# Kernel tuning notes

Hardware: AMD Instinct MI355X
Metric: run time of the kernel (lower is better)

The kernel has to match this reference:

```python
import jax, jax.numpy as jnp
import numpy as np

NS, B, PH = 8, 1024, 12
XS, ZS, RNN = 256, 32, 512
LS, LPS = 8, 2           # len_state, len_pred_state
IN = LPS + ZS + XS       # GRU input size (include_robot=False)
DT = 0.4                 # SingleIntegrator dt


def setup_inputs() -> dict:
    key = jax.random.key(0)
    ks = jax.random.split(key, 16)
    g = lambda k, sh, s=0.05: jax.random.normal(k, sh, dtype=jnp.float32) * s
    N = NS * B
    return {
        "x": g(ks[0], (B, XS), 1.0),
        "x_r_t0": g(ks[1], (B, LS), 1.0),
        "z_stacked": g(ks[2], (NS, B, ZS), 1.0),
        "p0": g(ks[3], (B, 2), 1.0),
        "eps_step": g(ks[4], (PH, N, 2), 1.0),
        "eps_final": g(ks[5], (NS, B, PH, 2), 1.0),
        "W_sa": g(ks[6], (LPS, LS)), "b_sa": jnp.zeros((LPS,), jnp.float32),
        "W_ih": g(ks[7], (3 * RNN, IN)), "b_ih": jnp.zeros((3 * RNN,), jnp.float32),
        "W_hh": g(ks[8], (3 * RNN, RNN)), "b_hh": jnp.zeros((3 * RNN,), jnp.float32),
        "W_h0": g(ks[9], (RNN, ZS + XS)), "b_h0": jnp.zeros((RNN,), jnp.float32),
        "W_mu": g(ks[10], (LPS, RNN)), "b_mu": jnp.zeros((LPS,), jnp.float32),
        "W_ls": g(ks[11], (LPS, RNN), 0.01), "b_ls": jnp.zeros((LPS,), jnp.float32),
        "W_corr": g(ks[12], (1, RNN), 0.01), "b_corr": jnp.zeros((1,), jnp.float32),
        "prediction_horizon": PH,
        "n_samples": NS,
    }


def _gmm_sample(mus, log_sigmas, rho, eps):
    # Reparameterized sample from a single-component 2D correlated Gaussian:
    # a = mu + L @ eps with L = [[sx, 0], [sy*rho, sy*sqrt(1-rho^2)]]
    s = jnp.exp(log_sigmas)
    dx = s[..., 0] * eps[..., 0]
    dy = s[..., 1] * (rho * eps[..., 0]
                      + jnp.sqrt(jnp.clip(1.0 - rho * rho, 1e-5, None)) * eps[..., 1])
    return mus + jnp.stack([dx, dy], axis=-1)


def reference(x, x_r_t0, z_stacked, p0, eps_step, eps_final,
              W_sa, b_sa, W_ih, b_ih, W_hh, b_hh, W_h0, b_h0,
              W_mu, b_mu, W_ls, b_ls, W_corr, b_corr,
              prediction_horizon, n_samples):
    ns, bsz, zs = z_stacked.shape
    z = z_stacked.reshape(-1, zs)                               # [N, z]
    zx = jnp.concatenate([z, jnp.tile(x, (n_samples, 1))], axis=1)  # [N, z+x]
    state0 = zx @ W_h0.T + b_h0                                 # initial_h
    a0 = jnp.tile(x_r_t0 @ W_sa.T + b_sa, (n_samples, 1))       # state_action

    def step(carry, eps_t):
        h, a = carry
        inp = jnp.concatenate([zx, a], axis=1)                  # [N, IN]
        gi = inp @ W_ih.T + b_ih
        gh = h @ W_hh.T + b_hh
        ir, iz, inn = jnp.split(gi, 3, axis=1)
        hr, hz, hn = jnp.split(gh, 3, axis=1)
        r = jax.nn.sigmoid(ir + hr)
        u = jax.nn.sigmoid(iz + hz)
        n = jnp.tanh(inn + r * hn)
        h_new = (1.0 - u) * n + u * h                           # GRUCell
        mus = h_new @ W_mu.T + b_mu                             # [N, 2]
        log_sigmas = h_new @ W_ls.T + b_ls                      # [N, 2]
        corrs = jnp.tanh(h_new @ W_corr.T + b_corr)[:, 0]       # [N]
        a_t = _gmm_sample(mus, log_sigmas, corrs, eps_t)        # gmm.rsample()
        return (h_new, a_t), (mus, log_sigmas, corrs)

    _, (mus, log_sigmas, corrs) = jax.lax.scan(step, (state0, a0), eps_step)
    # [PH, N, .] -> [n_samples, B, PH, .]  (n_components == 1)
    mus = mus.transpose(1, 0, 2).reshape(n_samples, bsz, prediction_horizon, 2)
    log_sigmas = log_sigmas.transpose(1, 0, 2).reshape(n_samples, bsz, prediction_horizon, 2)
    corrs = corrs.transpose(1, 0).reshape(n_samples, bsz, prediction_horizon, 1)
    log_pis = jnp.ones_like(corrs)                              # ones_like path (n_components==1)

    # a_dist.rsample() then SingleIntegrator.integrate_samples
    a_sample = _gmm_sample(mus, log_sigmas, corrs[..., 0], eps_final)
    preds = jnp.cumsum(a_sample, axis=2) * DT + p0[None, :, None, :]
    return (log_pis, mus, log_sigmas, corrs, preds)
```

## Files before the change

kernel.cpp:

```cpp
#include <hip/hip_runtime.h>
#include <hip/hip_bf16.h>
#include <math.h>

#define NSAMP 8
#define BATCH 1024
#define PH 12
#define XS 256
#define ZS 32
#define RNN 512
#define LSZ 8
#define INP 290
#define NTOT 8192
#define DT 0.4f

#define LOGPI_OFF 0
#define MUS_OFF   (NTOT*PH)
#define LSIG_OFF  (MUS_OFF + NTOT*PH*2)
#define CORR_OFF  (LSIG_OFF + NTOT*PH*2)
#define PRED_OFF  (CORR_OFF + NTOT*PH)

typedef float f32x4 __attribute__((ext_vector_type(4)));
typedef __bf16 bf16x8 __attribute__((ext_vector_type(8)));

__device__ __forceinline__ float sigmoid_(float x) {
    return 1.0f / (1.0f + __expf(-x));
}
__device__ __forceinline__ float tanh_(float x) {
    return 1.0f - 2.0f / (__expf(2.0f * x) + 1.0f);
}
__device__ __forceinline__ unsigned short f2bfu(float v) {
    __hip_bfloat16 b = __float2bfloat16(v);
    return __builtin_bit_cast(unsigned short, b);
}

__device__ __forceinline__ void async16(const void* g, void* l) {
    __builtin_amdgcn_global_load_lds((const __attribute__((address_space(1))) void*)g,
                                     (__attribute__((address_space(3))) void*)l, 16, 0, 0);
}


__global__ void k_init_a(const float* __restrict__ x_r_t0,
                         const float* __restrict__ W_sa,
                         const float* __restrict__ b_sa,
                         float* __restrict__ a) {
    int n = blockIdx.x * blockDim.x + threadIdx.x;
    if (n >= NTOT) return;
    int b = n & (BATCH - 1);
    float a0 = b_sa[0], a1 = b_sa[1];
#pragma unroll
    for (int k = 0; k < LSZ; ++k) {
        float xv = x_r_t0[b * LSZ + k];
        a0 = fmaf(xv, W_sa[0 * LSZ + k], a0);
        a1 = fmaf(xv, W_sa[1 * LSZ + k], a1);
    }
    a[n * 2 + 0] = a0;
    a[n * 2 + 1] = a1;
}

__global__ void k_cast_zx(const float* __restrict__ z, const float* __restrict__ x,
                          __hip_bfloat16* __restrict__ zx) {
    int n = blockIdx.x, k = threadIdx.x;
    if (k >= 288) return;
    float v = (k < 32) ? z[n * ZS + k] : x[(n & (BATCH - 1)) * XS + (k - 32)];
    zx[(size_t)n * 288 + k] = __float2bfloat16(v);
}

__global__ void k_cast_w(const float* __restrict__ W_h0, const float* __restrict__ W_ih,
                         __hip_bfloat16* __restrict__ Wcat) {
    int r = blockIdx.x, k = threadIdx.x;
    if (k >= 288) return;
    float v = (r < RNN) ? W_h0[r * 288 + k] : W_ih[(size_t)(r - RNN) * INP + k];
    Wcat[(size_t)r * 288 + k] = __float2bfloat16(v);
}

__global__ void k_cast_whh(const float* __restrict__ W, __hip_bfloat16* __restrict__ Wb) {
    int i = blockIdx.x * 256 + threadIdx.x;
    Wb[i] = __float2bfloat16(W[i]);
}

__global__ __launch_bounds__(256, 2) void k_gemm0_mfma(
    const __hip_bfloat16* __restrict__ zx, const __hip_bfloat16* __restrict__ Wcat,
    const float* __restrict__ b_h0, const float* __restrict__ b_ih,
    __hip_bfloat16* __restrict__ h0, unsigned short* __restrict__ giP)
{
    __shared__ __align__(16) char sA[8192];
    __shared__ __align__(16) char sB[8192];
    const int tid = threadIdx.x;
    const int wv = tid >> 6, lane = tid & 63;
    const int fq = lane >> 4, fr = lane & 15;
    const int wr = wv >> 1, wc = wv & 1;
    const int tile_r = blockIdx.x * 128, tile_c = blockIdx.y * 128;

    f32x4 acc[4][4];
#pragma unroll
    for (int i = 0; i < 4; ++i)
#pragma unroll
        for (int j = 0; j < 4; ++j) acc[i][j] = (f32x4){0.f, 0.f, 0.f, 0.f};

    for (int k0 = 0; k0 < 288; k0 += 32) {
#pragma unroll
        for (int j = 0; j < 2; ++j) {
            int ck = wv * 2 + j;
            int row = ck * 16 + (lane >> 2);
            int slot = lane & 3;
            async16(zx + (size_t)(tile_r + row) * 288 + k0 + ((slot ^ (row & 3)) << 3),
                    sA + ck * 1024 + lane * 16);
        }
#pragma unroll
        for (int j = 0; j < 2; ++j) {
            int ck = wv * 2 + j;
            int row = ck * 16 + (lane >> 2);
            int slot = lane & 3;
            async16(Wcat + (size_t)(tile_c + row) * 288 + k0 + ((slot ^ (row & 3)) << 3),
                    sB + ck * 1024 + lane * 16);
        }
        __syncthreads();
        bf16x8 af[4], bv[4];
#pragma unroll
        for (int i = 0; i < 4; ++i) {
            int r = wr * 64 + i * 16 + fr;
            af[i] = *(const bf16x8*)(sA + r * 64 + ((fq ^ (r & 3)) << 4));
        }
#pragma unroll
        for (int j = 0; j < 4; ++j) {
            int r = wc * 64 + j * 16 + fr;
            bv[j] = *(const bf16x8*)(sB + r * 64 + ((fq ^ (r & 3)) << 4));
        }
#pragma unroll
        for (int i = 0; i < 4; ++i)
#pragma unroll
            for (int j = 0; j < 4; ++j)
                acc[i][j] = __builtin_amdgcn_mfma_f32_16x16x32_bf16(af[i], bv[j], acc[i][j], 0, 0, 0);
        __syncthreads();
    }

#pragma unroll
    for (int jn = 0; jn < 4; ++jn) {
        const int cg_full = tile_c + wc * 64 + jn * 16 + fr;
        if (cg_full < RNN) {
            const float bias = b_h0[cg_full];
#pragma unroll
            for (int i = 0; i < 4; ++i)
#pragma unroll
                for (int q = 0; q < 4; ++q) {
                    int rg = tile_r + wr * 64 + i * 16 + fq * 4 + q;
                    h0[(size_t)rg * RNN + cg_full] = __float2bfloat16(acc[i][jn][q] + bias);
                }
        } else {
            const int cp = cg_full - RNN;
            const float bias = b_ih[cp];
            const int g = cp >> 9;
            const int cgm = cp & 511;
            const int by = cgm >> 6;
            const int wcg = (cgm >> 5) & 1;
            const int jg = (cgm >> 4) & 1;
            const int frg = cgm & 15;
#pragma unroll
            for (int i = 0; i < 4; ++i) {
                const int rg = tile_r + wr * 64 + i * 16 + fq * 4;
                const int bxg = rg >> 8;
                const int r255 = rg & 255;
                const int wrg = r255 >> 6;
                const int ig = (r255 >> 4) & 3;
                const int fqg = (r255 >> 2) & 3;
                const int tidg = (wrg * 2 + wcg) * 64 + fqg * 16 + frg;
                const size_t base = ((size_t)(bxg * 8 + by) * 512 + tidg) * 96
                                    + (jg * 3 + g) * 16 + ig * 4;
                ushort4 pk;
                pk.x = f2bfu(acc[i][jn][0] + bias);
                pk.y = f2bfu(acc[i][jn][1] + bias);
                pk.z = f2bfu(acc[i][jn][2] + bias);
                pk.w = f2bfu(acc[i][jn][3] + bias);
                *reinterpret_cast<ushort4*>(giP + base) = pk;
            }
        }
    }
}

#define GRU_LDS_A 32768
#define GRU_LDS_BUF 57344
__global__ __launch_bounds__(512, 2) void k_gru_step_mfma(
    const __hip_bfloat16* __restrict__ h, const float* __restrict__ a,
    const unsigned short* __restrict__ giP,
    const __hip_bfloat16* __restrict__ Whh, const float* __restrict__ b_hh,
    const float* __restrict__ W_ih,
    __hip_bfloat16* __restrict__ h_new)
{
    __shared__ __align__(16) char lds[2][GRU_LDS_BUF];
    const int tid = threadIdx.x;
    const int wv = tid >> 6, lane = tid & 63;
    const int fq = lane >> 4, fr = lane & 15;
    const int wr = wv >> 1, wc = wv & 1;
    const int tile_r = blockIdx.x * 256;
    const int tile_c = blockIdx.y * 64;

    const unsigned short* pg = giP + ((size_t)(blockIdx.x * 8 + blockIdx.y) * 512 + tid) * 96;
    bf16x8 gv[12];
#pragma unroll
    for (int e = 0; e < 12; ++e)
        gv[e] = *reinterpret_cast<const bf16x8*>(pg + e * 8);

    f32x4 acc[3][4][2];
#pragma unroll
    for (int g = 0; g < 3; ++g)
#pragma unroll
        for (int i = 0; i < 4; ++i)
#pragma unroll
            for (int j = 0; j < 2; ++j) acc[g][i][j] = (f32x4){0.f, 0.f, 0.f, 0.f};

    const int lrow = lane >> 2;
    const int slot = (lane & 3) ^ (lrow & 3);

    auto stage = [&](int b, int k0) {
#pragma unroll
        for (int j = 0; j < 7; ++j) {
            int c = wv * 7 + j;
            if (c < 32) {
                int rowgrp = c >> 1, kh = c & 1;
                int row = tile_r + rowgrp * 16 + lrow;
                async16(h + (size_t)row * RNN + k0 + kh * 32 + slot * 8,
                        lds[b] + c * 1024 + lane * 16);
            } else {
                int cp = c - 32;
                int grp = cp >> 1, kh = cp & 1;
                int rB = grp * 16 + lrow;
                int gate = rB >> 6, col = rB & 63;
                async16(Whh + (size_t)(gate * RNN + tile_c + col) * RNN + k0 + kh * 32 + slot * 8,
                        lds[b] + GRU_LDS_A + cp * 1024 + lane * 16);
            }
        }
    };

    auto compute = [&](int b) {
        const char* bufA = lds[b];
        const char* bufB = lds[b] + GRU_LDS_A;
        const int rsw = (fq ^ (fr & 3)) << 4;
#pragma unroll
        for (int ks = 0; ks < 2; ++ks) {
            bf16x8 af[4];
#pragma unroll
            for (int i = 0; i < 4; ++i) {
                int chunk = (wr * 4 + i) * 2 + ks;
                af[i] = *(const bf16x8*)(bufA + chunk * 1024 + fr * 64 + rsw);
            }
            bf16x8 bv[3][2];
#pragma unroll
            for (int g = 0; g < 3; ++g)
#pragma unroll
                for (int j = 0; j < 2; ++j) {
                    int grp = g * 4 + wc * 2 + j;
                    int chunk = grp * 2 + ks;
                    bv[g][j] = *(const bf16x8*)(bufB + chunk * 1024 + fr * 64 + rsw);
                }
#pragma unroll
            for (int g = 0; g < 3; ++g)
#pragma unroll
                for (int i = 0; i < 4; ++i)
#pragma unroll
                    for (int j = 0; j < 2; ++j)
                        acc[g][i][j] = __builtin_amdgcn_mfma_f32_16x16x32_bf16(
                            af[i], bv[g][j], acc[g][i][j], 0, 0, 0);
        }
    };

    stage(0, 0);
    __syncthreads();
    int buf = 0;
#pragma unroll 1
    for (int t = 0; t < 7; ++t) {
        stage(buf ^ 1, (t + 1) * 64);
        compute(buf);
        __syncthreads();
        buf ^= 1;
    }
    compute(buf);

#pragma unroll
    for (int j = 0; j < 2; ++j) {
        const int cg = tile_c + wc * 32 + j * 16 + fr;
        const float bh_r = b_hh[cg], bh_z = b_hh[RNN + cg], bh_n = b_hh[2 * RNN + cg];
        const float wr0 = W_ih[(size_t)cg * INP + 288],             wr1 = W_ih[(size_t)cg * INP + 289];
        const float wz0 = W_ih[(size_t)(RNN + cg) * INP + 288],     wz1 = W_ih[(size_t)(RNN + cg) * INP + 289];
        const float wn0 = W_ih[(size_t)(2 * RNN + cg) * INP + 288], wn1 = W_ih[(size_t)(2 * RNN + cg) * INP + 289];
#pragma unroll
        for (int i = 0; i < 4; ++i)
#pragma unroll
            for (int q = 0; q < 4; ++q) {
                const int rg = tile_r + wr * 64 + i * 16 + fq * 4 + q;
                const int idx = i * 4 + q;
                const int half = idx >> 3, lidx = idx & 7;
                const float2 av = *(const float2*)&a[rg * 2];
                const float gr = __bfloat162float(gv[(j * 3 + 0) * 2 + half][lidx])
                                 + av.x * wr0 + av.y * wr1 + acc[0][i][j][q] + bh_r;
                const float gz = __bfloat162float(gv[(j * 3 + 1) * 2 + half][lidx])
                                 + av.x * wz0 + av.y * wz1 + acc[1][i][j][q] + bh_z;
                const float gn = __bfloat162float(gv[(j * 3 + 2) * 2 + half][lidx])
                                 + av.x * wn0 + av.y * wn1;
                const float r_ = sigmoid_(gr);
                const float u_ = sigmoid_(gz);
                const float n_ = tanh_(gn + r_ * (acc[2][i][j][q] + bh_n));
                const float hv = __bfloat162float(h[(size_t)rg * RNN + cg]);
                h_new[(size_t)rg * RNN + cg] = __float2bfloat16((1.0f - u_) * n_ + u_ * hv);
            }
    }
}

__global__ __launch_bounds__(256) void k_heads(
    const __hip_bfloat16* __restrict__ h_new,
    const float* __restrict__ W_mu, const float* __restrict__ b_mu,
    const float* __restrict__ W_ls, const float* __restrict__ b_ls,
    const float* __restrict__ W_corr, const float* __restrict__ b_corr,
    const float* __restrict__ eps_step_t,
    float* __restrict__ out, float* __restrict__ a, int t)
{
    const int wid = (blockIdx.x * blockDim.x + threadIdx.x) >> 6;
    const int lane = threadIdx.x & 63;
    if (wid >= NTOT) return;
    const int kbase = lane * 8;
    float hv[8];
    {
        uint4 v = *reinterpret_cast<const uint4*>(&h_new[(size_t)wid * RNN + kbase]);
        unsigned uu[4] = {v.x, v.y, v.z, v.w};
#pragma unroll
        for (int p = 0; p < 4; ++p) {
            hv[2 * p]     = __uint_as_float(uu[p] << 16);
            hv[2 * p + 1] = __uint_as_float(uu[p] & 0xffff0000u);
        }
    }
    float s0 = 0.f, s1 = 0.f, s2 = 0.f, s3 = 0.f, s4 = 0.f;
#pragma unroll
    for (int q = 0; q < 8; ++q) {
        int k = kbase + q;
        s0 = fmaf(hv[q], W_mu[k], s0);
        s1 = fmaf(hv[q], W_mu[RNN + k], s1);
        s2 = fmaf(hv[q], W_ls[k], s2);
        s3 = fmaf(hv[q], W_ls[RNN + k], s3);
        s4 = fmaf(hv[q], W_corr[k], s4);
    }
#pragma unroll
    for (int m = 32; m >= 1; m >>= 1) {
        s0 += __shfl_xor(s0, m, 64);
        s1 += __shfl_xor(s1, m, 64);
        s2 += __shfl_xor(s2, m, 64);
        s3 += __shfl_xor(s3, m, 64);
        s4 += __shfl_xor(s4, m, 64);
    }
    if (lane == 0) {
        const int n = wid;
        const float mu0 = s0 + b_mu[0], mu1 = s1 + b_mu[1];
        const float ls0 = s2 + b_ls[0], ls1 = s3 + b_ls[1];
        const float rho = tanh_(s4 + b_corr[0]);
        out[MUS_OFF + (n * PH + t) * 2 + 0] = mu0;
        out[MUS_OFF + (n * PH + t) * 2 + 1] = mu1;
        out[LSIG_OFF + (n * PH + t) * 2 + 0] = ls0;
        out[LSIG_OFF + (n * PH + t) * 2 + 1] = ls1;
        out[CORR_OFF + n * PH + t] = rho;
        const float e0 = eps_step_t[n * 2 + 0], e1 = eps_step_t[n * 2 + 1];
        const float sg0 = __expf(ls0), sg1 = __expf(ls1);
        a[n * 2 + 0] = mu0 + sg0 * e0;
        a[n * 2 + 1] = mu1 + sg1 * (rho * e0 + sqrtf(fmaxf(1e-5f, 1.0f - rho * rho)) * e1);
    }
}

__global__ void k_final(const float* __restrict__ p0,
                        const float* __restrict__ eps_final,
                        float* __restrict__ out)
{
    int n = blockIdx.x * blockDim.x + threadIdx.x;
    if (n >= NTOT) return;
    const int b = n & (BATCH - 1);
    const float px = p0[b * 2 + 0], py = p0[b * 2 + 1];
    float cx = 0.f, cy = 0.f;
#pragma unroll
    for (int t = 0; t < PH; ++t) {
        const float mu0 = out[MUS_OFF + (n * PH + t) * 2 + 0];
        const float mu1 = out[MUS_OFF + (n * PH + t) * 2 + 1];
        const float ls0 = out[LSIG_OFF + (n * PH + t) * 2 + 0];
        const float ls1 = out[LSIG_OFF + (n * PH + t) * 2 + 1];
        const float rho = out[CORR_OFF + n * PH + t];
        const float e0 = eps_final[(n * PH + t) * 2 + 0];
        const float e1 = eps_final[(n * PH + t) * 2 + 1];
        const float sg0 = __expf(ls0), sg1 = __expf(ls1);
        cx += mu0 + sg0 * e0;
        cy += mu1 + sg1 * (rho * e0 + sqrtf(fmaxf(1e-5f, 1.0f - rho * rho)) * e1);
        out[PRED_OFF + (n * PH + t) * 2 + 0] = cx * DT + px;
        out[PRED_OFF + (n * PH + t) * 2 + 1] = cy * DT + py;
        out[LOGPI_OFF + n * PH + t] = 1.0f;
    }
}

extern "C" void kernel_launch(void* const* d_in, const int* in_sizes, int n_in,
                              void* d_out, int out_size, void* d_ws, size_t ws_size,
                              hipStream_t stream) {
    const float* x        = (const float*)d_in[0];
    const float* x_r_t0   = (const float*)d_in[1];
    const float* z        = (const float*)d_in[2];
    const float* p0       = (const float*)d_in[3];
    const float* eps_step = (const float*)d_in[4];
    const float* eps_fin  = (const float*)d_in[5];
    const float* W_sa     = (const float*)d_in[6];
    const float* b_sa     = (const float*)d_in[7];
    const float* W_ih     = (const float*)d_in[8];
    const float* b_ih     = (const float*)d_in[9];
    const float* W_hh     = (const float*)d_in[10];
    const float* b_hh     = (const float*)d_in[11];
    const float* W_h0     = (const float*)d_in[12];
    const float* b_h0     = (const float*)d_in[13];
    const float* W_mu     = (const float*)d_in[14];
    const float* b_mu     = (const float*)d_in[15];
    const float* W_ls     = (const float*)d_in[16];
    const float* b_ls     = (const float*)d_in[17];
    const float* W_corr   = (const float*)d_in[18];
    const float* b_corr   = (const float*)d_in[19];

    char* wp = (char*)d_ws;
    float* a            = (float*)wp;          wp += (size_t)NTOT * 2 * 4;
    __hip_bfloat16* zxb = (__hip_bfloat16*)wp; wp += (size_t)NTOT * 288 * 2;
    __hip_bfloat16* Wcat= (__hip_bfloat16*)wp; wp += (size_t)2048 * 288 * 2;
    __hip_bfloat16* Whhb= (__hip_bfloat16*)wp; wp += (size_t)1536 * RNN * 2;
    __hip_bfloat16* h0  = (__hip_bfloat16*)wp; wp += (size_t)NTOT * RNN * 2;
    __hip_bfloat16* h1  = (__hip_bfloat16*)wp; wp += (size_t)NTOT * RNN * 2;
    unsigned short* giP = (unsigned short*)wp; wp += (size_t)NTOT * 1536 * 2;
    float* out = (float*)d_out;

    k_init_a<<<dim3(NTOT / 256), dim3(256), 0, stream>>>(x_r_t0, W_sa, b_sa, a);
    k_cast_zx<<<dim3(NTOT), dim3(320), 0, stream>>>(z, x, zxb);
    k_cast_w<<<dim3(2048), dim3(320), 0, stream>>>(W_h0, W_ih, Wcat);
    k_cast_whh<<<dim3(1536 * RNN / 256), dim3(256), 0, stream>>>(W_hh, Whhb);
    k_gemm0_mfma<<<dim3(64, 16), dim3(256), 0, stream>>>(zxb, Wcat, b_h0, b_ih, h0, giP);

    __hip_bfloat16* hc = h0;
    __hip_bfloat16* hn = h1;
    for (int t = 0; t < PH; ++t) {
        k_gru_step_mfma<<<dim3(NTOT / 256, RNN / 64), dim3(512), 0, stream>>>(
            hc, a, giP, Whhb, b_hh, W_ih, hn);
        k_heads<<<dim3(NTOT * 64 / 256), dim3(256), 0, stream>>>(
            hn, W_mu, b_mu, W_ls, b_ls, W_corr, b_corr,
            eps_step + (size_t)t * NTOT * 2, out, a, t);
        __hip_bfloat16* tmp = hc; hc = hn; hn = tmp;
    }
    k_final<<<dim3(NTOT / 256), dim3(256), 0, stream>>>(p0, eps_fin, out);
}
```

Measured before the change: 426.0 us.

## Restructure GRU step K-loop with deeper prefetch and explicit waitcnt barriers

Replaces the double-buffered __syncthreads loop in the GRU MFMA step kernel with a fully unrolled loop. Two stages are prefetched ahead, LDS fragments are read into registers before a barrier so the freed buffer can be refilled early, and explicit vmcnt/lgkmcnt waits replace full syncs. MFMA issue is wrapped in s_setprio, and the gate-input register loads move after the GEMM loop to lower register pressure during it. This relies on the hand-set vmcnt(7) matching the per-thread load count (7 async loads per stage), which may be fragile. Holding all fragments in registers also raises register use.

Result: slower. 480.6 us (+12.8%).

```diff
diff --git a/kernel.cpp b/kernel.cpp
--- a/kernel.cpp
+++ b/kernel.cpp
@@ -21,6 +21,12 @@
 
 typedef float f32x4 __attribute__((ext_vector_type(4)));
 typedef __bf16 bf16x8 __attribute__((ext_vector_type(8)));
+
+#define ASM_VMCNT7() asm volatile("s_waitcnt vmcnt(7)" ::: "memory")
+#define ASM_VMCNT0() asm volatile("s_waitcnt vmcnt(0)" ::: "memory")
+#define ASM_LGKM0()  asm volatile("s_waitcnt lgkmcnt(0)" ::: "memory")
+#define SBAR()       __builtin_amdgcn_s_barrier()
+#define SCHEDB()     __builtin_amdgcn_sched_barrier(0)
 
 __device__ __forceinline__ float sigmoid_(float x) {
     return 1.0f / (1.0f + __expf(-x));
@@ -194,12 +200,6 @@
     const int tile_r = blockIdx.x * 256;
     const int tile_c = blockIdx.y * 64;
 
-    const unsigned short* pg = giP + ((size_t)(blockIdx.x * 8 + blockIdx.y) * 512 + tid) * 96;
-    bf16x8 gv[12];
-#pragma unroll
-    for (int e = 0; e < 12; ++e)
-        gv[e] = *reinterpret_cast<const bf16x8*>(pg + e * 8);
-
     f32x4 acc[3][4][2];
 #pragma unroll
     for (int g = 0; g < 3; ++g)
@@ -231,27 +231,34 @@
         }
     };
 
-    auto compute = [&](int b) {
+    bf16x8 af[4][2];
+    bf16x8 bv[3][2][2];
+    const int rsw = (fq ^ (fr & 3)) << 4;
+
+    auto ldsread = [&](int b) {
         const char* bufA = lds[b];
         const char* bufB = lds[b] + GRU_LDS_A;
-        const int rsw = (fq ^ (fr & 3)) << 4;
 #pragma unroll
         for (int ks = 0; ks < 2; ++ks) {
-            bf16x8 af[4];
 #pragma unroll
             for (int i = 0; i < 4; ++i) {
                 int chunk = (wr * 4 + i) * 2 + ks;
-                af[i] = *(const bf16x8*)(bufA + chunk * 1024 + fr * 64 + rsw);
+                af[i][ks] = *(const bf16x8*)(bufA + chunk * 1024 + fr * 64 + rsw);
             }
-            bf16x8 bv[3][2];
 #pragma unroll
             for (int g = 0; g < 3; ++g)
 #pragma unroll
                 for (int j = 0; j < 2; ++j) {
                     int grp = g * 4 + wc * 2 + j;
                     int chunk = grp * 2 + ks;
-                    bv[g][j] = *(const bf16x8*)(bufB + chunk * 1024 + fr * 64 + rsw);
+                    bv[g][j][ks] = *(const bf16x8*)(bufB + chunk * 1024 + fr * 64 + rsw);
                 }
+        }
+    };
+
+    auto domfma = [&]() {
+#pragma unroll
+        for (int ks = 0; ks < 2; ++ks)
 #pragma unroll
             for (int g = 0; g < 3; ++g)
 #pragma unroll
@@ -259,21 +266,38 @@
 #pragma unroll
                     for (int j = 0; j < 2; ++j)
                         acc[g][i][j] = __builtin_amdgcn_mfma_f32_16x16x32_bf16(
-                            af[i], bv[g][j], acc[g][i][j], 0, 0, 0);
-        }
+                            af[i][ks], bv[g][j][ks], acc[g][i][j], 0, 0, 0);
     };
 
     stage(0, 0);
-    __syncthreads();
-    int buf = 0;
-#pragma unroll 1
-    for (int t = 0; t < 7; ++t) {
-        stage(buf ^ 1, (t + 1) * 64);
-        compute(buf);
-        __syncthreads();
-        buf ^= 1;
-    }
-    compute(buf);
+    stage(1, 64);
+    ASM_VMCNT7();
+    SBAR();
+    SCHEDB();
+
+#pragma unroll
+    for (int t = 0; t < 8; ++t) {
+        ldsread(t & 1);
+        ASM_LGKM0();
+        SCHEDB();
+        SBAR();
+        if (t + 2 < 8) stage(t & 1, (t + 2) * 64);
+        __builtin_amdgcn_s_setprio(1);
+        domfma();
+        __builtin_amdgcn_s_setprio(0);
+        if (t < 7) {
+            if (t + 2 < 8) ASM_VMCNT7();
+            else           ASM_VMCNT0();
+            SBAR();
+            SCHEDB();
+        }
+    }
+
+    const unsigned short* pg = giP + ((size_t)(blockIdx.x * 8 + blockIdx.y) * 512 + tid) * 96;
+    bf16x8 gv[12];
+#pragma unroll
+    for (int e = 0; e < 12; ++e)
+        gv[e] = *reinterpret_cast<const bf16x8*>(pg + e * 8);
 
 #pragma unroll
     for (int j = 0; j < 2; ++j) {
```

## Deepen GRU-step prefetch pipeline, double-buffer gemm0, and merge prep kernels

Applied to the files above, without the earlier changes.

The GRU step kernel now stages two K-tiles ahead and uses explicit vmcnt/lgkmcnt waits with raw barriers in place of full __syncthreads. It also defers the giP gate-input loads until after the matmul loop, which frees registers during the main loop. The initial gemm0 kernel gains double-buffered LDS so the next tile loads while the current one computes. The four small prep/cast kernels are merged into two to cut launch overhead. The hand-placed waitcnt logic is fragile if the number of outstanding loads per thread changes.

Result: slower. 485.0 us (+13.8%).

```diff
diff --git a/kernel.cpp b/kernel.cpp
--- a/kernel.cpp
+++ b/kernel.cpp
@@ -22,6 +22,11 @@
 typedef float f32x4 __attribute__((ext_vector_type(4)));
 typedef __bf16 bf16x8 __attribute__((ext_vector_type(8)));
 
+#define ASM_VMCNT7() asm volatile("s_waitcnt vmcnt(7)" ::: "memory")
+#define ASM_VMCNT0() asm volatile("s_waitcnt vmcnt(0)" ::: "memory")
+#define ASM_LGKM0()  asm volatile("s_waitcnt lgkmcnt(0)" ::: "memory")
+#define SBAR()       __builtin_amdgcn_s_barrier()
+
 __device__ __forceinline__ float sigmoid_(float x) {
     return 1.0f / (1.0f + __expf(-x));
 }
@@ -38,44 +43,41 @@
                                      (__attribute__((address_space(3))) void*)l, 16, 0, 0);
 }
 
-
-__global__ void k_init_a(const float* __restrict__ x_r_t0,
-                         const float* __restrict__ W_sa,
-                         const float* __restrict__ b_sa,
-                         float* __restrict__ a) {
-    int n = blockIdx.x * blockDim.x + threadIdx.x;
-    if (n >= NTOT) return;
-    int b = n & (BATCH - 1);
-    float a0 = b_sa[0], a1 = b_sa[1];
-#pragma unroll
-    for (int k = 0; k < LSZ; ++k) {
-        float xv = x_r_t0[b * LSZ + k];
-        a0 = fmaf(xv, W_sa[0 * LSZ + k], a0);
-        a1 = fmaf(xv, W_sa[1 * LSZ + k], a1);
-    }
-    a[n * 2 + 0] = a0;
-    a[n * 2 + 1] = a1;
-}
-
-__global__ void k_cast_zx(const float* __restrict__ z, const float* __restrict__ x,
-                          __hip_bfloat16* __restrict__ zx) {
+__global__ void k_prep1(const float* __restrict__ z, const float* __restrict__ x,
+                        const float* __restrict__ x_r_t0,
+                        const float* __restrict__ W_sa, const float* __restrict__ b_sa,
+                        __hip_bfloat16* __restrict__ zx, float* __restrict__ a) {
     int n = blockIdx.x, k = threadIdx.x;
-    if (k >= 288) return;
-    float v = (k < 32) ? z[n * ZS + k] : x[(n & (BATCH - 1)) * XS + (k - 32)];
-    zx[(size_t)n * 288 + k] = __float2bfloat16(v);
-}
-
-__global__ void k_cast_w(const float* __restrict__ W_h0, const float* __restrict__ W_ih,
-                         __hip_bfloat16* __restrict__ Wcat) {
-    int r = blockIdx.x, k = threadIdx.x;
-    if (k >= 288) return;
-    float v = (r < RNN) ? W_h0[r * 288 + k] : W_ih[(size_t)(r - RNN) * INP + k];
-    Wcat[(size_t)r * 288 + k] = __float2bfloat16(v);
-}
-
-__global__ void k_cast_whh(const float* __restrict__ W, __hip_bfloat16* __restrict__ Wb) {
-    int i = blockIdx.x * 256 + threadIdx.x;
-    Wb[i] = __float2bfloat16(W[i]);
+    if (k < 288) {
+        float v = (k < 32) ? z[n * ZS + k] : x[(n & (BATCH - 1)) * XS + (k - 32)];
+        zx[(size_t)n * 288 + k] = __float2bfloat16(v);
+    } else if (k == 288) {
+        int b = n & (BATCH - 1);
+        float a0 = b_sa[0], a1 = b_sa[1];
+#pragma unroll
+        for (int kk = 0; kk < LSZ; ++kk) {
+            float xv = x_r_t0[b * LSZ + kk];
+            a0 = fmaf(xv, W_sa[0 * LSZ + kk], a0);
+            a1 = fmaf(xv, W_sa[1 * LSZ + kk], a1);
+        }
+        a[n * 2 + 0] = a0;
+        a[n * 2 + 1] = a1;
+    }
+}
+
+__global__ void k_prep2(const float* __restrict__ W_h0, const float* __restrict__ W_ih,
+                        const float* __restrict__ W_hh,
+                        __hip_bfloat16* __restrict__ Wcat, __hip_bfloat16* __restrict__ Whhb) {
+    int bid = blockIdx.x;
+    if (bid < 2048) {
+        int r = bid, k = threadIdx.x;
+        if (k >= 288) return;
+        float v = (r < RNN) ? W_h0[r * 288 + k] : W_ih[(size_t)(r - RNN) * INP + k];
+        Wcat[(size_t)r * 288 + k] = __float2bfloat16(v);
+    } else {
+        int i = (bid - 2048) * 320 + threadIdx.x;
+        if (i < 1536 * RNN) Whhb[i] = __float2bfloat16(W_hh[i]);
+    }
 }
 
 __global__ __launch_bounds__(256, 2) void k_gemm0_mfma(
@@ -83,8 +85,7 @@
     const float* __restrict__ b_h0, const float* __restrict__ b_ih,
     __hip_bfloat16* __restrict__ h0, unsigned short* __restrict__ giP)
 {
-    __shared__ __align__(16) char sA[8192];
-    __shared__ __align__(16) char sB[8192];
+    __shared__ __align__(16) char sAB[2][16384];
     const int tid = threadIdx.x;
     const int wv = tid >> 6, lane = tid & 63;
     const int fq = lane >> 4, fr = lane & 15;
@@ -97,14 +98,14 @@
 #pragma unroll
         for (int j = 0; j < 4; ++j) acc[i][j] = (f32x4){0.f, 0.f, 0.f, 0.f};
 
-    for (int k0 = 0; k0 < 288; k0 += 32) {
+    auto stage = [&](int b, int k0) {
 #pragma unroll
         for (int j = 0; j < 2; ++j) {
             int ck = wv * 2 + j;
             int row = ck * 16 + (lane >> 2);
             int slot = lane & 3;
             async16(zx + (size_t)(tile_r + row) * 288 + k0 + ((slot ^ (row & 3)) << 3),
-                    sA + ck * 1024 + lane * 16);
+                    sAB[b] + ck * 1024 + lane * 16);
         }
 #pragma unroll
         for (int j = 0; j < 2; ++j) {
@@ -112,26 +113,38 @@
             int row = ck * 16 + (lane >> 2);
             int slot = lane & 3;
             async16(Wcat + (size_t)(tile_c + row) * 288 + k0 + ((slot ^ (row & 3)) << 3),
-                    sB + ck * 1024 + lane * 16);
-        }
-        __syncthreads();
+                    sAB[b] + 8192 + ck * 1024 + lane * 16);
+        }
+    };
+
+    auto compute = [&](int b) {
         bf16x8 af[4], bv[4];
 #pragma unroll
         for (int i = 0; i < 4; ++i) {
             int r = wr * 64 + i * 16 + fr;
-            af[i] = *(const bf16x8*)(sA + r * 64 + ((fq ^ (r & 3)) << 4));
+            af[i] = *(const bf16x8*)(sAB[b] + r * 64 + ((fq ^ (r & 3)) << 4));
         }
 #pragma unroll
         for (int j = 0; j < 4; ++j) {
             int r = wc * 64 + j * 16 + fr;
-            bv[j] = *(const bf16x8*)(sB + r * 64 + ((fq ^ (r & 3)) << 4));
+            bv[j] = *(const bf16x8*)(sAB[b] + 8192 + r * 64 + ((fq ^ (r & 3)) << 4));
         }
 #pragma unroll
         for (int i = 0; i < 4; ++i)
 #pragma unroll
             for (int j = 0; j < 4; ++j)
                 acc[i][j] = __builtin_amdgcn_mfma_f32_16x16x32_bf16(af[i], bv[j], acc[i][j], 0, 0, 0);
+    };
+
+    stage(0, 0);
+    __syncthreads();
+    int buf = 0;
+#pragma unroll 1
+    for (int t = 0; t < 9; ++t) {
+        if (t < 8) stage(buf ^ 1, (t + 1) * 32);
+        compute(buf);
         __syncthreads();
+        buf ^= 1;
     }
 
 #pragma unroll
@@ -194,12 +207,6 @@
     const int tile_r = blockIdx.x * 256;
     const int tile_c = blockIdx.y * 64;
 
-    const unsigned short* pg = giP + ((size_t)(blockIdx.x * 8 + blockIdx.y) * 512 + tid) * 96;
-    bf16x8 gv[12];
-#pragma unroll
-    for (int e = 0; e < 12; ++e)
-        gv[e] = *reinterpret_cast<const bf16x8*>(pg + e * 8);
-
     f32x4 acc[3][4][2];
 #pragma unroll
     for (int g = 0; g < 3; ++g)
@@ -210,6 +217,7 @@
 
     const int lrow = lane >> 2;
     const int slot = (lane & 3) ^ (lrow & 3);
+    const int rsw = (fq ^ (fr & 3)) << 4;
 
     auto stage = [&](int b, int k0) {
 #pragma unroll
@@ -231,49 +239,57 @@
         }
     };
 
-    auto compute = [&](int b) {
+    auto half = [&](int b, int ks) {
         const char* bufA = lds[b];
         const char* bufB = lds[b] + GRU_LDS_A;
-        const int rsw = (fq ^ (fr & 3)) << 4;
-#pragma unroll
-        for (int ks = 0; ks < 2; ++ks) {
-            bf16x8 af[4];
-#pragma unroll
-            for (int i = 0; i < 4; ++i) {
-                int chunk = (wr * 4 + i) * 2 + ks;
-                af[i] = *(const bf16x8*)(bufA + chunk * 1024 + fr * 64 + rsw);
-            }
-            bf16x8 bv[3][2];
-#pragma unroll
-            for (int g = 0; g < 3; ++g)
-#pragma unroll
-                for (int j = 0; j < 2; ++j) {
-                    int grp = g * 4 + wc * 2 + j;
-                    int chunk = grp * 2 + ks;
-                    bv[g][j] = *(const bf16x8*)(bufB + chunk * 1024 + fr * 64 + rsw);
-                }
-#pragma unroll
-            for (int g = 0; g < 3; ++g)
-#pragma unroll
-                for (int i = 0; i < 4; ++i)
-#pragma unroll
-                    for (int j = 0; j < 2; ++j)
-                        acc[g][i][j] = __builtin_amdgcn_mfma_f32_16x16x32_bf16(
-                            af[i], bv[g][j], acc[g][i][j], 0, 0, 0);
-        }
+        bf16x8 af[4];
+#pragma unroll
+        for (int i = 0; i < 4; ++i)
+            af[i] = *(const bf16x8*)(bufA + ((wr * 4 + i) * 2 + ks) * 1024 + fr * 64 + rsw);
+        bf16x8 bv[3][2];
+#pragma unroll
+        for (int g = 0; g < 3; ++g)
+#pragma unroll
+            for (int j = 0; j < 2; ++j)
+                bv[g][j] = *(const bf16x8*)(bufB + ((g * 4 + wc * 2 + j) * 2 + ks) * 1024 + fr * 64 + rsw);
+#pragma unroll
+        for (int g = 0; g < 3; ++g)
+#pragma unroll
+            for (int i = 0; i < 4; ++i)
+#pragma unroll
+                for (int j = 0; j < 2; ++j)
+                    acc[g][i][j] = __builtin_amdgcn_mfma_f32_16x16x32_bf16(
+                        af[i], bv[g][j], acc[g][i][j], 0, 0, 0);
     };
 
     stage(0, 0);
-    __syncthreads();
+    stage(1, 64);
+    ASM_VMCNT7();
+    SBAR();
+
     int buf = 0;
 #pragma unroll 1
-    for (int t = 0; t < 7; ++t) {
-        stage(buf ^ 1, (t + 1) * 64);
-        compute(buf);
-        __syncthreads();
+    for (int t = 0; t < 8; ++t) {
+        half(buf, 0);
+        half(buf, 1);
+        ASM_LGKM0();
+        SBAR();
+        if (t + 2 < 8) {
+            stage(buf, (t + 2) * 64);
+            ASM_VMCNT7();
+            SBAR();
+        } else if (t < 7) {
+            ASM_VMCNT0();
+            SBAR();
+        }
         buf ^= 1;
     }
-    compute(buf);
+
+    const unsigned short* pg = giP + ((size_t)(blockIdx.x * 8 + blockIdx.y) * 512 + tid) * 96;
+    bf16x8 gv[12];
+#pragma unroll
+    for (int e = 0; e < 12; ++e)
+        gv[e] = *reinterpret_cast<const bf16x8*>(pg + e * 8);
 
 #pragma unroll
     for (int j = 0; j < 2; ++j) {
@@ -288,13 +304,13 @@
             for (int q = 0; q < 4; ++q) {
                 const int rg = tile_r + wr * 64 + i * 16 + fq * 4 + q;
                 const int idx = i * 4 + q;
-                const int half = idx >> 3, lidx = idx & 7;
+                const int half_ = idx >> 3, lidx = idx & 7;
                 const float2 av = *(const float2*)&a[rg * 2];
-                const float gr = __bfloat162float(gv[(j * 3 + 0) * 2 + half][lidx])
+                const float gr = __bfloat162float(gv[(j * 3 + 0) * 2 + half_][lidx])
                                  + av.x * wr0 + av.y * wr1 + acc[0][i][j][q] + bh_r;
-                const float gz = __bfloat162float(gv[(j * 3 + 1) * 2 + half][lidx])
+                const float gz = __bfloat162float(gv[(j * 3 + 1) * 2 + half_][lidx])
                                  + av.x * wz0 + av.y * wz1 + acc[1][i][j][q] + bh_z;
-                const float gn = __bfloat162float(gv[(j * 3 + 2) * 2 + half][lidx])
+                const float gn = __bfloat162float(gv[(j * 3 + 2) * 2 + half_][lidx])
                                  + av.x * wn0 + av.y * wn1;
                 const float r_ = sigmoid_(gr);
                 const float u_ = sigmoid_(gz);
@@ -423,10 +439,8 @@
     unsigned short* giP = (unsigned short*)wp; wp += (size_t)NTOT * 1536 * 2;
     float* out = (float*)d_out;
 
-    k_init_a<<<dim3(NTOT / 256), dim3(256), 0, stream>>>(x_r_t0, W_sa, b_sa, a);
-    k_cast_zx<<<dim3(NTOT), dim3(320), 0, stream>>>(z, x, zxb);
-    k_cast_w<<<dim3(2048), dim3(320), 0, stream>>>(W_h0, W_ih, Wcat);
-    k_cast_whh<<<dim3(1536 * RNN / 256), dim3(256), 0, stream>>>(W_hh, Whhb);
+    k_prep1<<<dim3(NTOT), dim3(320), 0, stream>>>(z, x, x_r_t0, W_sa, b_sa, zxb, a);
+    k_prep2<<<dim3(5120), dim3(320), 0, stream>>>(W_h0, W_ih, W_hh, Wcat, Whhb);
     k_gemm0_mfma<<<dim3(64, 16), dim3(256), 0, stream>>>(zxb, Wcat, b_h0, b_ih, h0, giP);
 
     __hip_bfloat16* hc = h0;
```
